# Performance work log

Hardware: AMD Instinct MI355X
Metric: run time of the kernel (lower is better)

## Reference

```python
import jax, jax.numpy as jnp
import numpy as np

WINDOW = (8, 8)
NUM_HEADS = 12


def setup_inputs() -> dict:
    key = jax.random.key(0)
    k0, k1, k2 = jax.random.split(key, 3)
    B_, H, W, C = 8, 64, 64, 768
    x = jax.random.normal(k0, (B_, H * W, C), dtype=jnp.float32)
    qkv_w = jax.random.normal(k1, (3 * C, C), dtype=jnp.float32) * 0.02
    qkv_b = jnp.zeros((3 * C,), dtype=jnp.float32)
    proj_w = jax.random.normal(k2, (C, C), dtype=jnp.float32) * 0.02
    proj_b = jnp.zeros((C,), dtype=jnp.float32)
    return {"x": x, "qkv_w": qkv_w, "qkv_b": qkv_b,
            "proj_w": proj_w, "proj_b": proj_b, "H": H, "W": W}


def reference(x, qkv_w, qkv_b, proj_w, proj_b, H, W):
    ws0, ws1 = WINDOW
    nh = NUM_HEADS
    B_, N, C = x.shape
    hd = C // nh
    scale = hd ** (-0.5)

    x = x.reshape(B_, H, W, C)
    # pad bottom/right so H, W divisible by window size (static Python ints)
    pad_b = (ws0 - H % ws0) % ws0
    pad_r = (ws1 - W % ws1) % ws1
    x = jnp.pad(x, ((0, 0), (0, pad_b), (0, pad_r), (0, 0)))
    Hp, Wp = H + pad_b, W + pad_r

    # window partition: (B, Hp, Wp, C) -> (B*nW, ws0*ws1, C)
    xw = (x.reshape(B_, Hp // ws0, ws0, Wp // ws1, ws1, C)
            .transpose(0, 1, 3, 2, 4, 5)
            .reshape(-1, ws0 * ws1, C))
    Bw, Nw = xw.shape[0], xw.shape[1]

    # fused qkv projection
    qkv = xw @ qkv_w.T + qkv_b                       # (Bw, Nw, 3C)
    qkv = qkv.reshape(Bw, Nw, 3, nh, hd).transpose(2, 0, 3, 1, 4)
    q, k, v = qkv[0], qkv[1], qkv[2]                 # (Bw, nh, Nw, hd)

    attn = jax.nn.softmax((q * scale) @ jnp.swapaxes(k, -2, -1), axis=-1)
    out = (attn @ v).transpose(0, 2, 1, 3).reshape(Bw, Nw, C)
    out = out @ proj_w.T + proj_b

    # window reverse: (B*nW, ws0*ws1, C) -> (B, Hp, Wp, C)
    out = (out.reshape(B_, Hp // ws0, Wp // ws1, ws0, ws1, C)
              .transpose(0, 1, 3, 2, 4, 5)
              .reshape(B_, Hp, Wp, C))
    out = out[:, :H, :W, :]
    return out.reshape(B_, H * W, C)
```

## Files before the change

### kernel.cpp

```cpp
#include <hip/hip_runtime.h>
#include <stdint.h>

typedef __attribute__((ext_vector_type(8))) __bf16 bf16x8;
typedef __attribute__((ext_vector_type(4))) float f32x4;
typedef __attribute__((ext_vector_type(8))) unsigned short u16x8;

__device__ __forceinline__ unsigned short f2bf(float f) {
  union { float f; unsigned u; } v; v.f = f;
  return (unsigned short)((v.u + 0x7FFFu + ((v.u >> 16) & 1u)) >> 16);
}

__device__ __forceinline__ void gload16(const void* g, void* l) {
  __builtin_amdgcn_global_load_lds(
      (const __attribute__((address_space(1))) void*)g,
      (__attribute__((address_space(3))) void*)l, 16, 0, 0);
}

__global__ __launch_bounds__(256) void pack_x_kernel(const float* __restrict__ x,
                                                     unsigned short* __restrict__ xw) {
  int idx = blockIdx.x * 256 + threadIdx.x;
  int m = idx / 96;
  int p = idx - m * 96;
  int win = m >> 6, tok = m & 63;
  int b = win >> 6, wh = (win >> 3) & 7, ww = win & 7;
  int r = tok >> 3, c = tok & 7;
  size_t xoff = ((size_t)b * 4096 + (wh * 8 + r) * 64 + (ww * 8 + c)) * 768 + p * 8;
  const float* src = x + xoff;
  u16x8 o;
#pragma unroll
  for (int j = 0; j < 8; ++j) o[j] = f2bf(src[j]);
  *(u16x8*)(xw + (size_t)m * 768 + p * 8) = o;
}

__global__ __launch_bounds__(256) void pack_w_kernel(const float* __restrict__ qkvw,
                                                     const float* __restrict__ projw,
                                                     unsigned short* __restrict__ wq,
                                                     unsigned short* __restrict__ wp) {
  int idx = blockIdx.x * 256 + threadIdx.x;
  const float* src;
  unsigned short* dst;
  if (idx < 221184) { src = qkvw + (size_t)idx * 8; dst = wq + (size_t)idx * 8; }
  else { int i2 = idx - 221184; src = projw + (size_t)i2 * 8; dst = wp + (size_t)i2 * 8; }
  u16x8 o;
#pragma unroll
  for (int j = 0; j < 8; ++j) o[j] = f2bf(src[j]);
  *(u16x8*)dst = o;
}

__global__ __launch_bounds__(256) void gemm_qkv_kernel(
    const unsigned short* __restrict__ A, const unsigned short* __restrict__ B,
    const float* __restrict__ bias, unsigned short* __restrict__ C) {
  constexpr int K = 768;
  constexpr int N = 2304;
  __shared__ unsigned short sA[128 * 32];
  __shared__ unsigned short sB[128 * 32];
  const int tid = threadIdx.x;
  const int wave = tid >> 6;
  const int lane = tid & 63;
  const int tm = (blockIdx.x / (N / 128)) * 128;
  const int tn = (blockIdx.x % (N / 128)) * 128;

  const int sr = tid >> 2;
  const int skb = (tid & 3) * 8;
  const unsigned short* gA = A + (size_t)(tm + sr) * K + skb;
  const unsigned short* gB = B + (size_t)(tn + sr) * K + skb;
  char* lA = (char*)sA + wave * 1024;
  char* lB = (char*)sB + wave * 1024;

  const int wr = (wave >> 1) * 64;
  const int wc = (wave & 1) * 64;
  const int lrow = lane & 15;
  const int lkb = (lane >> 4) * 8;

  f32x4 acc[4][4] = {};

  for (int k0 = 0; k0 < K; k0 += 32) {
    __syncthreads();
    gload16(gA + k0, lA);
    gload16(gA + k0 + (size_t)64 * K, lA + 4096);
    gload16(gB + k0, lB);
    gload16(gB + k0 + (size_t)64 * K, lB + 4096);
    __syncthreads();
    bf16x8 af[4], bfv[4];
#pragma unroll
    for (int mi = 0; mi < 4; ++mi)
      af[mi] = *(const bf16x8*)&sA[(wr + mi * 16 + lrow) * 32 + lkb];
#pragma unroll
    for (int ni = 0; ni < 4; ++ni)
      bfv[ni] = *(const bf16x8*)&sB[(wc + ni * 16 + lrow) * 32 + lkb];
#pragma unroll
    for (int mi = 0; mi < 4; ++mi)
#pragma unroll
      for (int ni = 0; ni < 4; ++ni)
        acc[mi][ni] = __builtin_amdgcn_mfma_f32_16x16x32_bf16(af[mi], bfv[ni], acc[mi][ni], 0, 0, 0);
  }

  const int crow = tm + wr + ((lane >> 4) << 2);
  const int ccol = tn + wc + lrow;
#pragma unroll
  for (int ni = 0; ni < 4; ++ni) {
    const int col = ccol + ni * 16;
    const float bv = bias[col];
#pragma unroll
    for (int mi = 0; mi < 4; ++mi)
#pragma unroll
      for (int r = 0; r < 4; ++r)
        C[(size_t)(crow + mi * 16 + r) * N + col] = f2bf(acc[mi][ni][r] + bv);
  }
}

__global__ __launch_bounds__(64) void attn_kernel(const unsigned short* __restrict__ qkv,
                                                  unsigned short* __restrict__ attnout) {
  __shared__ unsigned short sQ[64 * 64];
  __shared__ unsigned short sK[64 * 64];
  __shared__ unsigned short sVT[64 * 64];
  const int lane = threadIdx.x;
  const int win = blockIdx.x / 12;
  const int head = blockIdx.x - win * 12;
  const size_t row0 = (size_t)win * 64;
  const int qoff = head * 64, koff = 768 + head * 64, voff = 1536 + head * 64;

#pragma unroll
  for (int i = 0; i < 8; ++i) {
    int e = lane + i * 64;
    int row = e >> 3, cb = (e & 7) * 8;
    gload16(qkv + (row0 + row) * 2304 + qoff + cb, (char*)sQ + i * 1024);
    gload16(qkv + (row0 + row) * 2304 + koff + cb, (char*)sK + i * 1024);
  }
  {
    const unsigned short* gv = qkv + (row0 + lane) * 2304 + voff;
#pragma unroll
    for (int j = 0; j < 8; ++j) {
      u16x8 v = *(const u16x8*)(gv + j * 8);
#pragma unroll
      for (int d = 0; d < 8; ++d) sVT[(j * 8 + d) * 64 + lane] = v[d];
    }
  }
  __syncthreads();

  const int lrow = lane & 15;
  const int lkb = (lane >> 4) * 8;

  f32x4 s[4][4] = {};
#pragma unroll
  for (int ks = 0; ks < 2; ++ks) {
    bf16x8 qf[4], kf[4];
#pragma unroll
    for (int mi = 0; mi < 4; ++mi) qf[mi] = *(const bf16x8*)&sQ[(mi * 16 + lrow) * 64 + ks * 32 + lkb];
#pragma unroll
    for (int ni = 0; ni < 4; ++ni) kf[ni] = *(const bf16x8*)&sK[(ni * 16 + lrow) * 64 + ks * 32 + lkb];
#pragma unroll
    for (int mi = 0; mi < 4; ++mi)
#pragma unroll
      for (int ni = 0; ni < 4; ++ni)
        s[mi][ni] = __builtin_amdgcn_mfma_f32_16x16x32_bf16(qf[mi], kf[ni], s[mi][ni], 0, 0, 0);
  }

  float p[4][4][4];
#pragma unroll
  for (int mi = 0; mi < 4; ++mi) {
#pragma unroll
    for (int r = 0; r < 4; ++r) {
      float v0 = s[mi][0][r] * 0.125f, v1 = s[mi][1][r] * 0.125f;
      float v2 = s[mi][2][r] * 0.125f, v3 = s[mi][3][r] * 0.125f;
      float mx = fmaxf(fmaxf(v0, v1), fmaxf(v2, v3));
      mx = fmaxf(mx, __shfl_xor(mx, 1));
      mx = fmaxf(mx, __shfl_xor(mx, 2));
      mx = fmaxf(mx, __shfl_xor(mx, 4));
      mx = fmaxf(mx, __shfl_xor(mx, 8));
      float e0 = __expf(v0 - mx), e1 = __expf(v1 - mx);
      float e2 = __expf(v2 - mx), e3 = __expf(v3 - mx);
      float sm = e0 + e1 + e2 + e3;
      sm += __shfl_xor(sm, 1);
      sm += __shfl_xor(sm, 2);
      sm += __shfl_xor(sm, 4);
      sm += __shfl_xor(sm, 8);
      float inv = 1.0f / sm;
      p[mi][0][r] = e0 * inv; p[mi][1][r] = e1 * inv;
      p[mi][2][r] = e2 * inv; p[mi][3][r] = e3 * inv;
    }
  }

  __syncthreads();
#pragma unroll
  for (int mi = 0; mi < 4; ++mi)
#pragma unroll
    for (int ni = 0; ni < 4; ++ni)
#pragma unroll
      for (int r = 0; r < 4; ++r)
        sK[(mi * 16 + (lane >> 4) * 4 + r) * 64 + ni * 16 + lrow] = f2bf(p[mi][ni][r]);
  __syncthreads();

  f32x4 o[4][4] = {};
#pragma unroll
  for (int ks = 0; ks < 2; ++ks) {
    bf16x8 pf[4], vf[4];
#pragma unroll
    for (int mi = 0; mi < 4; ++mi) pf[mi] = *(const bf16x8*)&sK[(mi * 16 + lrow) * 64 + ks * 32 + lkb];
#pragma unroll
    for (int ni = 0; ni < 4; ++ni) vf[ni] = *(const bf16x8*)&sVT[(ni * 16 + lrow) * 64 + ks * 32 + lkb];
#pragma unroll
    for (int mi = 0; mi < 4; ++mi)
#pragma unroll
      for (int ni = 0; ni < 4; ++ni)
        o[mi][ni] = __builtin_amdgcn_mfma_f32_16x16x32_bf16(pf[mi], vf[ni], o[mi][ni], 0, 0, 0);
  }

#pragma unroll
  for (int mi = 0; mi < 4; ++mi)
#pragma unroll
    for (int ni = 0; ni < 4; ++ni) {
      int col = head * 64 + ni * 16 + lrow;
#pragma unroll
      for (int r = 0; r < 4; ++r) {
        int trow = mi * 16 + (lane >> 4) * 4 + r;
        attnout[(row0 + trow) * 768 + col] = f2bf(o[mi][ni][r]);
      }
    }
}

__global__ __launch_bounds__(256) void gemm_proj_kernel(
    const unsigned short* __restrict__ A, const unsigned short* __restrict__ B,
    const float* __restrict__ bias, float* __restrict__ out) {
  constexpr int K = 768;
  constexpr int N = 768;
  __shared__ unsigned short sA[128 * 32];
  __shared__ unsigned short sB[128 * 32];
  const int tid = threadIdx.x;
  const int wave = tid >> 6;
  const int lane = tid & 63;
  const int tm = (blockIdx.x / (N / 128)) * 128;
  const int tn = (blockIdx.x % (N / 128)) * 128;

  const int sr = tid >> 2;
  const int skb = (tid & 3) * 8;
  const unsigned short* gA = A + (size_t)(tm + sr) * K + skb;
  const unsigned short* gB = B + (size_t)(tn + sr) * K + skb;
  char* lA = (char*)sA + wave * 1024;
  char* lB = (char*)sB + wave * 1024;

  const int wr = (wave >> 1) * 64;
  const int wc = (wave & 1) * 64;
  const int lrow = lane & 15;
  const int lkb = (lane >> 4) * 8;

  f32x4 acc[4][4] = {};

  for (int k0 = 0; k0 < K; k0 += 32) {
    __syncthreads();
    gload16(gA + k0, lA);
    gload16(gA + k0 + (size_t)64 * K, lA + 4096);
    gload16(gB + k0, lB);
    gload16(gB + k0 + (size_t)64 * K, lB + 4096);
    __syncthreads();
    bf16x8 af[4], bfv[4];
#pragma unroll
    for (int mi = 0; mi < 4; ++mi)
      af[mi] = *(const bf16x8*)&sA[(wr + mi * 16 + lrow) * 32 + lkb];
#pragma unroll
    for (int ni = 0; ni < 4; ++ni)
      bfv[ni] = *(const bf16x8*)&sB[(wc + ni * 16 + lrow) * 32 + lkb];
#pragma unroll
    for (int mi = 0; mi < 4; ++mi)
#pragma unroll
      for (int ni = 0; ni < 4; ++ni)
        acc[mi][ni] = __builtin_amdgcn_mfma_f32_16x16x32_bf16(af[mi], bfv[ni], acc[mi][ni], 0, 0, 0);
  }

  const int crow = tm + wr + ((lane >> 4) << 2);
  const int ccol = tn + wc + lrow;
#pragma unroll
  for (int mi = 0; mi < 4; ++mi)
#pragma unroll
    for (int r = 0; r < 4; ++r) {
      int m = crow + mi * 16 + r;
      int win = m >> 6, tok = m & 63;
      int b = win >> 6, wh = (win >> 3) & 7, ww = win & 7;
      int rr = tok >> 3, cc = tok & 7;
      float* op = out + ((size_t)b * 4096 + (wh * 8 + rr) * 64 + (ww * 8 + cc)) * 768;
#pragma unroll
      for (int ni = 0; ni < 4; ++ni) {
        int col = ccol + ni * 16;
        op[col] = acc[mi][ni][r] + bias[col];
      }
    }
}

extern "C" void kernel_launch(void* const* d_in, const int* in_sizes, int n_in,
                              void* d_out, int out_size, void* d_ws, size_t ws_size,
                              hipStream_t stream) {
  (void)in_sizes; (void)n_in; (void)out_size; (void)ws_size;
  const float* x = (const float*)d_in[0];
  const float* qkv_w = (const float*)d_in[1];
  const float* qkv_b = (const float*)d_in[2];
  const float* proj_w = (const float*)d_in[3];
  const float* proj_b = (const float*)d_in[4];
  float* out = (float*)d_out;

  char* ws = (char*)d_ws;
  unsigned short* xw   = (unsigned short*)(ws);
  unsigned short* qkvB = (unsigned short*)(ws + 50331648);
  unsigned short* wq   = (unsigned short*)(ws + 50331648 + 150994944);
  unsigned short* wp   = (unsigned short*)(ws + 50331648 + 150994944 + 3538944);

  pack_x_kernel<<<12288, 256, 0, stream>>>(x, xw);
  pack_w_kernel<<<1152, 256, 0, stream>>>(qkv_w, proj_w, wq, wp);
  gemm_qkv_kernel<<<4608, 256, 0, stream>>>(xw, wq, qkv_b, qkvB);
  attn_kernel<<<6144, 64, 0, stream>>>(qkvB, xw);
  gemm_proj_kernel<<<1536, 256, 0, stream>>>(xw, wp, proj_b, out);
}
```

Before: 299.2 us.

## Replace GEMMs with 256x256-tile, 4-stage pipelined, swizzled-LDS templated kernel

```diff
diff --git a/kernel.cpp b/kernel.cpp
--- a/kernel.cpp
+++ b/kernel.cpp
@@ -47,65 +47,135 @@
   *(u16x8*)dst = o;
 }
 
-__global__ __launch_bounds__(256) void gemm_qkv_kernel(
-    const unsigned short* __restrict__ A, const unsigned short* __restrict__ B,
-    const float* __restrict__ bias, unsigned short* __restrict__ C) {
+template <int N, bool PROJ>
+__global__ __launch_bounds__(512) void gemm256_kernel(
+    const unsigned short* __restrict__ A, const unsigned short* __restrict__ Bm,
+    const float* __restrict__ bias, void* __restrict__ Cout) {
   constexpr int K = 768;
-  constexpr int N = 2304;
-  __shared__ unsigned short sA[128 * 32];
-  __shared__ unsigned short sB[128 * 32];
+  constexpr int NT = K / 32;
+  constexpr int NBN = N / 256;
+  extern __shared__ char smem[];
+
   const int tid = threadIdx.x;
   const int wave = tid >> 6;
   const int lane = tid & 63;
-  const int tm = (blockIdx.x / (N / 128)) * 128;
-  const int tn = (blockIdx.x % (N / 128)) * 128;
-
-  const int sr = tid >> 2;
-  const int skb = (tid & 3) * 8;
-  const unsigned short* gA = A + (size_t)(tm + sr) * K + skb;
-  const unsigned short* gB = B + (size_t)(tn + sr) * K + skb;
-  char* lA = (char*)sA + wave * 1024;
-  char* lB = (char*)sB + wave * 1024;
-
-  const int wr = (wave >> 1) * 64;
-  const int wc = (wave & 1) * 64;
+  const int wm = wave >> 2;
+  const int wn = wave & 3;
+
+  const int cpx = gridDim.x >> 3;
+  const int bid = (blockIdx.x & 7) * cpx + (blockIdx.x >> 3);
+  const int tm = (bid / NBN) * 256;
+  const int tn = (bid % NBN) * 256;
+
+  const int c0 = tid, c1 = 512 + tid;
+  const int r0 = c0 >> 2, r1 = c1 >> 2;
+  const int g0 = ((c0 & 3) ^ (r0 & 3)) * 8;
+  const int g1 = ((c1 & 3) ^ (r1 & 3)) * 8;
+  const unsigned short* gA0 = A + (size_t)(tm + r0) * K + g0;
+  const unsigned short* gA1 = A + (size_t)(tm + r1) * K + g1;
+  const unsigned short* gB0 = Bm + (size_t)(tn + r0) * K + g0;
+  const unsigned short* gB1 = Bm + (size_t)(tn + r1) * K + g1;
+  const int ldsA0 = wave * 1024;
+  const int ldsA1 = 8192 + wave * 1024;
+  const int ldsB0 = 16384 + wave * 1024;
+  const int ldsB1 = 16384 + 8192 + wave * 1024;
+
+  {
+    char* s0 = smem;
+    char* s1 = smem + 32768;
+    gload16(gA0, s0 + ldsA0); gload16(gA1, s0 + ldsA1);
+    gload16(gB0, s0 + ldsB0); gload16(gB1, s0 + ldsB1);
+    gload16(gA0 + 32, s1 + ldsA0); gload16(gA1 + 32, s1 + ldsA1);
+    gload16(gB0 + 32, s1 + ldsB0); gload16(gB1 + 32, s1 + ldsB1);
+  }
+  asm volatile("s_waitcnt vmcnt(4)" ::: "memory");
+  asm volatile("s_barrier" ::: "memory");
+
   const int lrow = lane & 15;
-  const int lkb = (lane >> 4) * 8;
-
-  f32x4 acc[4][4] = {};
-
-  for (int k0 = 0; k0 < K; k0 += 32) {
-    __syncthreads();
-    gload16(gA + k0, lA);
-    gload16(gA + k0 + (size_t)64 * K, lA + 4096);
-    gload16(gB + k0, lB);
-    gload16(gB + k0 + (size_t)64 * K, lB + 4096);
-    __syncthreads();
-    bf16x8 af[4], bfv[4];
-#pragma unroll
-    for (int mi = 0; mi < 4; ++mi)
-      af[mi] = *(const bf16x8*)&sA[(wr + mi * 16 + lrow) * 32 + lkb];
+  const int lg8 = ((lane >> 4) ^ (lane & 3)) * 8;
+
+  f32x4 acc[8][4] = {};
+
+  for (int t = 0; t < NT; ++t) {
+    const unsigned short* sAt = (const unsigned short*)(smem + ((t & 3) << 15));
+    const unsigned short* sBt = sAt + 8192;
+
+    bf16x8 a[4], b[4];
+#pragma unroll
+    for (int mi = 0; mi < 4; ++mi)
+      a[mi] = *(const bf16x8*)(sAt + (wm * 128 + mi * 16 + lrow) * 32 + lg8);
 #pragma unroll
     for (int ni = 0; ni < 4; ++ni)
-      bfv[ni] = *(const bf16x8*)&sB[(wc + ni * 16 + lrow) * 32 + lkb];
+      b[ni] = *(const bf16x8*)(sBt + (wn * 64 + ni * 16 + lrow) * 32 + lg8);
+    if (t + 2 < NT) {
+      char* sb = smem + (((t + 2) & 3) << 15);
+      gload16(gA0 + (t + 2) * 32, sb + ldsA0);
+      gload16(gA1 + (t + 2) * 32, sb + ldsA1);
+    }
+    asm volatile("s_barrier" ::: "memory");
+    __builtin_amdgcn_s_setprio(1);
 #pragma unroll
     for (int mi = 0; mi < 4; ++mi)
 #pragma unroll
       for (int ni = 0; ni < 4; ++ni)
-        acc[mi][ni] = __builtin_amdgcn_mfma_f32_16x16x32_bf16(af[mi], bfv[ni], acc[mi][ni], 0, 0, 0);
-  }
-
-  const int crow = tm + wr + ((lane >> 4) << 2);
-  const int ccol = tn + wc + lrow;
-#pragma unroll
-  for (int ni = 0; ni < 4; ++ni) {
-    const int col = ccol + ni * 16;
-    const float bv = bias[col];
-#pragma unroll
-    for (int mi = 0; mi < 4; ++mi)
-#pragma unroll
-      for (int r = 0; r < 4; ++r)
-        C[(size_t)(crow + mi * 16 + r) * N + col] = f2bf(acc[mi][ni][r] + bv);
+        acc[mi][ni] = __builtin_amdgcn_mfma_f32_16x16x32_bf16(a[mi], b[ni], acc[mi][ni], 0, 0, 0);
+    __builtin_amdgcn_s_setprio(0);
+    asm volatile("s_barrier" ::: "memory");
+
+#pragma unroll
+    for (int mi = 0; mi < 4; ++mi)
+      a[mi] = *(const bf16x8*)(sAt + (wm * 128 + 64 + mi * 16 + lrow) * 32 + lg8);
+    if (t + 2 < NT) {
+      char* sb = smem + (((t + 2) & 3) << 15);
+      gload16(gB0 + (t + 2) * 32, sb + ldsB0);
+      gload16(gB1 + (t + 2) * 32, sb + ldsB1);
+    }
+    if (t < NT - 2)
+      asm volatile("s_waitcnt vmcnt(4)" ::: "memory");
+    else if (t == NT - 2)
+      asm volatile("s_waitcnt vmcnt(0)" ::: "memory");
+    asm volatile("s_barrier" ::: "memory");
+    __builtin_amdgcn_s_setprio(1);
+#pragma unroll
+    for (int mi = 0; mi < 4; ++mi)
+#pragma unroll
+      for (int ni = 0; ni < 4; ++ni)
+        acc[4 + mi][ni] = __builtin_amdgcn_mfma_f32_16x16x32_bf16(a[mi], b[ni], acc[4 + mi][ni], 0, 0, 0);
+    __builtin_amdgcn_s_setprio(0);
+    asm volatile("s_barrier" ::: "memory");
+  }
+
+  const int crow = tm + wm * 128 + ((lane >> 4) << 2);
+  const int ccol0 = tn + wn * 64 + lrow;
+  if constexpr (!PROJ) {
+    unsigned short* C = (unsigned short*)Cout;
+#pragma unroll
+    for (int ni = 0; ni < 4; ++ni) {
+      const int col = ccol0 + ni * 16;
+      const float bv = bias[col];
+#pragma unroll
+      for (int mi = 0; mi < 8; ++mi)
+#pragma unroll
+        for (int r = 0; r < 4; ++r)
+          C[(size_t)(crow + mi * 16 + r) * N + col] = f2bf(acc[mi][ni][r] + bv);
+    }
+  } else {
+    float* out = (float*)Cout;
+#pragma unroll
+    for (int mi = 0; mi < 8; ++mi)
+#pragma unroll
+      for (int r = 0; r < 4; ++r) {
+        int m = crow + mi * 16 + r;
+        int win = m >> 6, tok = m & 63;
+        int bb = win >> 6, wh = (win >> 3) & 7, ww = win & 7;
+        int rr = tok >> 3, cc = tok & 7;
+        float* op = out + ((size_t)bb * 4096 + (wh * 8 + rr) * 64 + (ww * 8 + cc)) * 768;
+#pragma unroll
+        for (int ni = 0; ni < 4; ++ni) {
+          int col = ccol0 + ni * 16;
+          op[col] = acc[mi][ni][r] + bias[col];
+        }
+      }
   }
 }
 
@@ -219,73 +289,6 @@
     }
 }
 
-__global__ __launch_bounds__(256) void gemm_proj_kernel(
-    const unsigned short* __restrict__ A, const unsigned short* __restrict__ B,
-    const float* __restrict__ bias, float* __restrict__ out) {
-  constexpr int K = 768;
-  constexpr int N = 768;
-  __shared__ unsigned short sA[128 * 32];
-  __shared__ unsigned short sB[128 * 32];
-  const int tid = threadIdx.x;
-  const int wave = tid >> 6;
-  const int lane = tid & 63;
-  const int tm = (blockIdx.x / (N / 128)) * 128;
-  const int tn = (blockIdx.x % (N / 128)) * 128;
-
-  const int sr = tid >> 2;
-  const int skb = (tid & 3) * 8;
-  const unsigned short* gA = A + (size_t)(tm + sr) * K + skb;
-  const unsigned short* gB = B + (size_t)(tn + sr) * K + skb;
-  char* lA = (char*)sA + wave * 1024;
-  char* lB = (char*)sB + wave * 1024;
-
-  const int wr = (wave >> 1) * 64;
-  const int wc = (wave & 1) * 64;
-  const int lrow = lane & 15;
-  const int lkb = (lane >> 4) * 8;
-
-  f32x4 acc[4][4] = {};
-
-  for (int k0 = 0; k0 < K; k0 += 32) {
-    __syncthreads();
-    gload16(gA + k0, lA);
-    gload16(gA + k0 + (size_t)64 * K, lA + 4096);
-    gload16(gB + k0, lB);
-    gload16(gB + k0 + (size_t)64 * K, lB + 4096);
-    __syncthreads();
-    bf16x8 af[4], bfv[4];
-#pragma unroll
-    for (int mi = 0; mi < 4; ++mi)
-      af[mi] = *(const bf16x8*)&sA[(wr + mi * 16 + lrow) * 32 + lkb];
-#pragma unroll
-    for (int ni = 0; ni < 4; ++ni)
-      bfv[ni] = *(const bf16x8*)&sB[(wc + ni * 16 + lrow) * 32 + lkb];
-#pragma unroll
-    for (int mi = 0; mi < 4; ++mi)
-#pragma unroll
-      for (int ni = 0; ni < 4; ++ni)
-        acc[mi][ni] = __builtin_amdgcn_mfma_f32_16x16x32_bf16(af[mi], bfv[ni], acc[mi][ni], 0, 0, 0);
-  }
-
-  const int crow = tm + wr + ((lane >> 4) << 2);
-  const int ccol = tn + wc + lrow;
-#pragma unroll
-  for (int mi = 0; mi < 4; ++mi)
-#pragma unroll
-    for (int r = 0; r < 4; ++r) {
-      int m = crow + mi * 16 + r;
-      int win = m >> 6, tok = m & 63;
-      int b = win >> 6, wh = (win >> 3) & 7, ww = win & 7;
-      int rr = tok >> 3, cc = tok & 7;
-      float* op = out + ((size_t)b * 4096 + (wh * 8 + rr) * 64 + (ww * 8 + cc)) * 768;
-#pragma unroll
-      for (int ni = 0; ni < 4; ++ni) {
-        int col = ccol + ni * 16;
-        op[col] = acc[mi][ni][r] + bias[col];
-      }
-    }
-}
-
 extern "C" void kernel_launch(void* const* d_in, const int* in_sizes, int n_in,
                               void* d_out, int out_size, void* d_ws, size_t ws_size,
                               hipStream_t stream) {
@@ -303,9 +306,14 @@
   unsigned short* wq   = (unsigned short*)(ws + 50331648 + 150994944);
   unsigned short* wp   = (unsigned short*)(ws + 50331648 + 150994944 + 3538944);
 
+  (void)hipFuncSetAttribute((const void*)(gemm256_kernel<2304, false>),
+                            hipFuncAttributeMaxDynamicSharedMemorySize, 131072);
+  (void)hipFuncSetAttribute((const void*)(gemm256_kernel<768, true>),
+                            hipFuncAttributeMaxDynamicSharedMemorySize, 131072);
+
   pack_x_kernel<<<12288, 256, 0, stream>>>(x, xw);
   pack_w_kernel<<<1152, 256, 0, stream>>>(qkv_w, proj_w, wq, wp);
-  gemm_qkv_kernel<<<4608, 256, 0, stream>>>(xw, wq, qkv_b, qkvB);
+  gemm256_kernel<2304, false><<<1152, 512, 131072, stream>>>(xw, wq, qkv_b, qkvB);
   attn_kernel<<<6144, 64, 0, stream>>>(qkvB, xw);
-  gemm_proj_kernel<<<1536, 256, 0, stream>>>(xw, wp, proj_b, out);
-}
+  gemm256_kernel<768, true><<<384, 512, 131072, stream>>>(xw, wp, proj_b, out);
+}
```

Result: no change. 300.2 us (+0.3%).
